# Optimization experiments

Hardware: AMD Instinct MI355X
Metric: run time of the kernel (lower is better)

## Reference

```python
import jax, jax.numpy as jnp
import numpy as np

NUM_EXPERTS = 64
HIDDEN_DIM = 4096
TOPK = 8


def setup_inputs() -> dict:
    key = jax.random.key(0)
    kx, kw = jax.random.split(key)
    x = jax.random.normal(kx, (16384, HIDDEN_DIM), dtype=jnp.float32)
    # nn.Linear weight is [num_experts, hidden_dim], init N(0, 0.01)
    W = jax.random.normal(kw, (NUM_EXPERTS, HIDDEN_DIM), dtype=jnp.float32) * 0.01
    return {"x": x, "W": W}


def reference(x, W):
    # router logits: [T, E]
    router_logits = jnp.einsum('th,eh->te', x, W)
    score = jnp.clip(router_logits, -2.0, 2.0)
    # top-k over experts (no router_bias branch)
    topk_scores, topk_indices = jax.lax.top_k(score, TOPK)  # [T, K]
    topk_probs = jax.nn.softmax(topk_scores, axis=-1)
    # dispatch index computation (counting-sort style)
    flat = topk_indices.reshape(-1)                      # [T*K]
    indices = jnp.argsort(flat, stable=True).astype(jnp.int32)
    tokens_per_expert = jnp.bincount(flat, length=NUM_EXPERTS)
    group_indices = jnp.cumsum(tokens_per_expert).astype(jnp.int32)
    tokens_per_expert_f = tokens_per_expert.astype(jnp.float32)
    # load-balance loss
    mean_tokens = tokens_per_expert_f / tokens_per_expert_f.sum()
    mean_prob = jax.nn.softmax(router_logits, axis=-1).mean(axis=0)
    lb_loss = jnp.dot(mean_tokens, mean_prob) * NUM_EXPERTS
    # z-loss
    zl = jnp.mean(jax.scipy.special.logsumexp(router_logits, axis=-1) ** 2)
    return (router_logits, topk_probs, topk_indices, group_indices,
            indices, tokens_per_expert, lb_loss, zl)
```

## Files before the change

### kernel.cpp

```cpp
#include <hip/hip_runtime.h>
#include <hip/hip_bf16.h>
#include <math.h>

#define NTOK   16384
#define NEXP   64
#define HID    4096
#define KSEL   8
#define EPS    7.5e-5f
#define NSPLIT 4
#define KSZ    (HID / NSPLIT)

typedef __attribute__((ext_vector_type(8))) short short8;
typedef __attribute__((ext_vector_type(4))) float f32x4;

#define O_LOGITS 0u
#define O_PROBS  1048576u
#define O_TIDX   1179648u
#define O_GROUP  1310720u
#define O_IDX    1310784u
#define O_TPE    1441856u
#define O_LB     1441920u
#define O_ZL     1441921u

#define W_CQ      0u
#define W_GCOUNT  2048u
#define W_OFFS2   4096u
#define W_LSQP    8192u
#define W_LIST    16384u
#define W_PSUM    81920u
#define W_FLAT    262144u
#define W_WF      1048576u
#define W_PART    2097152u
#define PART_STRIDE 1048576ull

__device__ __forceinline__ unsigned short f2bf(float f) {
  unsigned u = __float_as_uint(f);
  return (unsigned short)((u + 0x7fffu + ((u >> 16) & 1u)) >> 16);
}

__device__ __forceinline__ void gload16(const void* g, void* l) {
  __builtin_amdgcn_global_load_lds((const __attribute__((address_space(1))) unsigned int*)g,
                                   (__attribute__((address_space(3))) unsigned int*)l, 16, 0, 0);
}

__global__ __launch_bounds__(256) void k_prep(const float* __restrict__ w,
                                              short8* __restrict__ wf,
                                              int* __restrict__ cq,
                                              int* __restrict__ gcount) {
  const int kk   = blockIdx.x;
  const int nb   = threadIdx.x >> 6;
  const int lane = threadIdx.x & 63;
  const int n    = nb * 16 + (lane & 15);
  const int kb   = kk * 32 + (lane >> 4) * 8;
  const float4* wp = (const float4*)(w + (size_t)n * HID + kb);
  float4 f0 = wp[0], f1 = wp[1];
  float fv[8] = {f0.x, f0.y, f0.z, f0.w, f1.x, f1.y, f1.z, f1.w};
  short8 hi, lo;
#pragma unroll
  for (int j = 0; j < 8; ++j) {
    unsigned short h = f2bf(fv[j]);
    hi[j] = (short)h;
    float r = fv[j] - __uint_as_float((unsigned)h << 16);
    lo[j] = (short)f2bf(r);
  }
  size_t base = ((size_t)(kk * 4 + nb) * 2) * 64 + lane;
  wf[base] = hi;
  wf[base + 64] = lo;
  if (blockIdx.x == 0) {
    cq[threadIdx.x] = 0;
    cq[threadIdx.x + 256] = 0;
    if (threadIdx.x == 0) gcount[0] = 0;
  }
}

__global__ __launch_bounds__(256, 4) void k_gemm(const float* __restrict__ x,
                                                 const short8* __restrict__ wf,
                                                 float* __restrict__ part) {
  __shared__ short8 wl[2][512];
  const int tid  = threadIdx.x;
  const int wv   = tid >> 6;
  const int lane = tid & 63;
  const int t0   = blockIdx.x * 64;
  const int k0   = blockIdx.y * KSZ;
  const int row  = t0 + wv * 16 + (lane & 15);

  const float* xp = x + (size_t)row * HID + k0 + (lane >> 4) * 8;
  const short8* wbase = wf + (size_t)(k0 >> 5) * 512;

  auto stage = [&](int c, int b) {
    const short8* src = wbase + (size_t)c * 512;
#pragma unroll
    for (int r = 0; r < 2; ++r) {
      const int o = r * 256 + wv * 64;
      gload16(src + o + lane, &wl[b][o]);
    }
  };

  f32x4 acc[4] = {{0,0,0,0},{0,0,0,0},{0,0,0,0},{0,0,0,0}};

  stage(0, 0);
  __syncthreads();
  const int nch = KSZ >> 5;
  for (int c = 0; c < nch; ++c) {
    const int b = c & 1;
    if (c + 1 < nch) stage(c + 1, b ^ 1);

    const float4* xq = (const float4*)(xp + c * 32);
    float4 f0 = xq[0], f1 = xq[1];
    unsigned xb[8] = {__float_as_uint(f0.x), __float_as_uint(f0.y),
                      __float_as_uint(f0.z), __float_as_uint(f0.w),
                      __float_as_uint(f1.x), __float_as_uint(f1.y),
                      __float_as_uint(f1.z), __float_as_uint(f1.w)};
    union { unsigned u[4]; short8 s; } ua, ul;
#pragma unroll
    for (int p = 0; p < 4; ++p) {
      unsigned b0 = xb[2 * p], b1 = xb[2 * p + 1];
      ua.u[p] = __builtin_amdgcn_perm(b1, b0, 0x07060302u);
      float r0 = __uint_as_float(b0) - __uint_as_float(b0 & 0xffff0000u);
      float r1 = __uint_as_float(b1) - __uint_as_float(b1 & 0xffff0000u);
      unsigned t0b = __float_as_uint(r0), t1b = __float_as_uint(r1);
      t0b += 0x7fffu + ((t0b >> 16) & 1u);
      t1b += 0x7fffu + ((t1b >> 16) & 1u);
      ul.u[p] = __builtin_amdgcn_perm(t1b, t0b, 0x07060302u);
    }
    short8 ah = ua.s, al = ul.s;

#pragma unroll
    for (int nb = 0; nb < 4; ++nb) {
      short8 bh = wl[b][nb * 128 + lane];
      short8 bl = wl[b][nb * 128 + 64 + lane];
      acc[nb] = __builtin_amdgcn_mfma_f32_16x16x32_bf16(ah, bh, acc[nb], 0, 0, 0);
      acc[nb] = __builtin_amdgcn_mfma_f32_16x16x32_bf16(al, bh, acc[nb], 0, 0, 0);
      acc[nb] = __builtin_amdgcn_mfma_f32_16x16x32_bf16(ah, bl, acc[nb], 0, 0, 0);
    }
    __syncthreads();
  }

  float* p = part + (size_t)blockIdx.y * PART_STRIDE;
  const int mrow = t0 + wv * 16 + (lane >> 4) * 4;
  const int col  = lane & 15;
#pragma unroll
  for (int nb = 0; nb < 4; ++nb)
#pragma unroll
    for (int r = 0; r < 4; ++r)
      p[(size_t)(mrow + r) * 64 + nb * 16 + col] = acc[nb][r];
}

__global__ __launch_bounds__(256) void k_rowtail(const float* __restrict__ part,
                                                 float* __restrict__ out,
                                                 int* __restrict__ cq,
                                                 float* __restrict__ psum,
                                                 float* __restrict__ lsqp,
                                                 int* __restrict__ gcount,
                                                 int* __restrict__ list,
                                                 int* __restrict__ flat) {
  __shared__ float tile[64][68];
  __shared__ float rmv[64], invv[64];
  __shared__ int   hist[64];
  const int bid  = blockIdx.x;
  const int tid  = threadIdx.x;
  const int wv   = tid >> 6;
  const int lane = tid & 63;
  const int t0   = bid * 64;
  if (tid < 64) hist[tid] = 0;

  {
    const size_t boff = (size_t)bid * 4096;
#pragma unroll
    for (int k = 0; k < 16; ++k) {
      int idx = k * 256 + tid;
      float v = part[boff + idx];
#pragma unroll
      for (int s = 1; s < NSPLIT; ++s) v += part[(size_t)s * PART_STRIDE + boff + idx];
      tile[idx >> 6][idx & 63] = v;
      out[O_LOGITS + boff + idx] = v;
    }
  }
  __syncthreads();

  if (wv == 1) {
    const int r = lane;
    float rm = -3.0e38f;
#pragma unroll
    for (int c4 = 0; c4 < 16; ++c4) {
      float4 f = *(float4*)&tile[r][c4 * 4];
      rm = fmaxf(rm, fmaxf(fmaxf(f.x, f.y), fmaxf(f.z, f.w)));
    }
    float se = 0.0f;
#pragma unroll
    for (int c4 = 0; c4 < 16; ++c4) {
      float4 f = *(float4*)&tile[r][c4 * 4];
      se += expf(f.x - rm) + expf(f.y - rm) + expf(f.z - rm) + expf(f.w - rm);
    }
    rmv[r] = rm; invv[r] = 1.0f / se;
    float lse = rm + logf(se);
    float l2 = lse * lse;
#pragma unroll
    for (int o = 32; o > 0; o >>= 1) l2 += __shfl_down(l2, o);
    if (lane == 0) lsqp[bid] = l2;
  }
  __syncthreads();

  if (wv == 0) {
    const unsigned t = t0 + lane;
    float val[9]; int idx[9];
#pragma unroll
    for (int j = 0; j < 9; ++j) { val[j] = -3.0e38f; idx[j] = 0; }
    bool flag = false;
#pragma unroll
    for (int c4 = 0; c4 < 16; ++c4) {
      float4 f = *(float4*)&tile[lane][c4 * 4];
      float fe[4] = {f.x, f.y, f.z, f.w};
#pragma unroll
      for (int jj = 0; jj < 4; ++jj) {
        float v = fe[jj];
        flag = flag || (fabsf(fabsf(v) - 2.0f) < EPS);
        float c = fminf(fmaxf(v, -2.0f), 2.0f);
        int id = c4 * 4 + jj;
#pragma unroll
        for (int j = 0; j < 9; ++j) {
          bool sw = c > val[j];
          float tv = sw ? val[j] : c; int ti = sw ? idx[j] : id;
          val[j] = sw ? c : val[j];   idx[j] = sw ? id : idx[j];
          c = tv; id = ti;
        }
      }
    }
#pragma unroll
    for (int j = 0; j < 8; ++j) {
      float gap = val[j] - val[j + 1];
      bool bothclip = (val[j] == val[j + 1]) && (fabsf(val[j]) == 2.0f);
      flag = flag || (gap < EPS && !bothclip);
    }
    if (!flag) {
      float m = val[0], pe[8], sum = 0.0f;
#pragma unroll
      for (int j = 0; j < 8; ++j) { pe[j] = expf(val[j] - m); sum += pe[j]; }
      float inv = 1.0f / sum;
      *(float4*)&out[O_PROBS + (size_t)t * 8]     = make_float4(pe[0]*inv, pe[1]*inv, pe[2]*inv, pe[3]*inv);
      *(float4*)&out[O_PROBS + (size_t)t * 8 + 4] = make_float4(pe[4]*inv, pe[5]*inv, pe[6]*inv, pe[7]*inv);
      *(float4*)&out[O_TIDX + (size_t)t * 8]      = make_float4((float)idx[0], (float)idx[1], (float)idx[2], (float)idx[3]);
      *(float4*)&out[O_TIDX + (size_t)t * 8 + 4]  = make_float4((float)idx[4], (float)idx[5], (float)idx[6], (float)idx[7]);
      *(int4*)&flat[(size_t)t * 8]     = make_int4(idx[0], idx[1], idx[2], idx[3]);
      *(int4*)&flat[(size_t)t * 8 + 4] = make_int4(idx[4], idx[5], idx[6], idx[7]);
#pragma unroll
      for (int j = 0; j < 8; ++j) atomicAdd(&hist[idx[j]], 1);
    } else {
      int sl = atomicAdd(gcount, 1);
      list[sl] = (int)t;
    }
  } else if (wv == 2 || wv == 3) {
    const int e = lane, half = wv - 2;
    float s = 0.0f;
#pragma unroll
    for (int r = 0; r < 32; ++r) {
      int rr = half * 32 + r;
      s += expf(tile[rr][e] - rmv[rr]) * invv[rr];
    }
    psum[(size_t)bid * 128 + half * 64 + e] = s;
  }
  __syncthreads();
  if (tid < 64) atomicAdd(&cq[(bid >> 5) * 64 + tid], hist[tid]);
}

__global__ __launch_bounds__(256) void k_repair(const float* __restrict__ x,
                                                const float* __restrict__ w,
                                                const int* __restrict__ list,
                                                const int* __restrict__ gcount,
                                                float* __restrict__ out,
                                                int* __restrict__ cq,
                                                int* __restrict__ flat) {
  __shared__ double sh[4][64];
  __shared__ double tot[64];
  const int tid = threadIdx.x;
  const int wave = tid >> 6, lane = tid & 63;
  const int n = *gcount;
  for (int i = blockIdx.x; i < n; i += 256) {
    const int row = list[i];
    const float* xr = x + (size_t)row * HID;
    const float* wr = w + (size_t)lane * HID;
    double p0 = 0.0, p1 = 0.0, p2 = 0.0, p3 = 0.0;
    const int kb = wave * 1024;
    for (int k = kb; k < kb + 1024; k += 4) {
      float4 xv = *(const float4*)&xr[k];
      float4 wv = *(const float4*)&wr[k];
      p0 = fma((double)xv.x, (double)wv.x, p0);
      p1 = fma((double)xv.y, (double)wv.y, p1);
      p2 = fma((double)xv.z, (double)wv.z, p2);
      p3 = fma((double)xv.w, (double)wv.w, p3);
    }
    sh[wave][lane] = (p0 + p1) + (p2 + p3);
    __syncthreads();
    if (wave == 0) tot[lane] = (sh[0][lane] + sh[1][lane]) + (sh[2][lane] + sh[3][lane]);
    __syncthreads();
    if (tid == 0) {
      double val[8]; int idx[8];
#pragma unroll
      for (int j = 0; j < 8; ++j) { val[j] = -1.0e300; idx[j] = 0; }
      for (int e = 0; e < 64; ++e) {
        double c = fmin(fmax(tot[e], -2.0), 2.0);
        int id = e;
#pragma unroll
        for (int j = 0; j < 8; ++j) {
          bool sw = c > val[j];
          double tv = sw ? val[j] : c; int ti = sw ? idx[j] : id;
          val[j] = sw ? c : val[j];    idx[j] = sw ? id : idx[j];
          c = tv; id = ti;
        }
      }
      float m = (float)val[0], pe[8], sum = 0.0f;
#pragma unroll
      for (int j = 0; j < 8; ++j) { pe[j] = expf((float)val[j] - m); sum += pe[j]; }
      float inv = 1.0f / sum;
      const int q = row >> 11;
#pragma unroll
      for (int j = 0; j < 8; ++j) {
        out[O_PROBS + (size_t)row * 8 + j] = pe[j] * inv;
        out[O_TIDX  + (size_t)row * 8 + j] = (float)idx[j];
        flat[(size_t)row * 8 + j] = idx[j];
        atomicAdd(&cq[q * 64 + idx[j]], 1);
      }
    }
    __syncthreads();
  }
}

__global__ __launch_bounds__(256) void k_final(const int* __restrict__ cq,
                                               const float* __restrict__ psum,
                                               const float* __restrict__ lsqp,
                                               float* __restrict__ out,
                                               int* __restrict__ offs2) {
  __shared__ int   ctot[64];
  __shared__ float gsum[4][64];
  const int tid = threadIdx.x;
  const int e = tid & 63, g = tid >> 6;

  if (tid < 64) {
    int tpe = 0;
#pragma unroll
    for (int q = 0; q < 8; ++q) tpe += cq[q * 64 + tid];
    ctot[tid] = tpe;
  }
  float ps = 0.0f;
  for (int b = g; b < 256; b += 4) ps += psum[(size_t)b * 128 + e] + psum[(size_t)b * 128 + 64 + e];
  gsum[g][e] = ps;
  __syncthreads();

  if (tid < 64) {
    int incl = 0;
    for (int i = 0; i <= tid; ++i) incl += ctot[i];
    int tpe = ctot[tid];
    out[O_TPE + tid]   = (float)tpe;
    out[O_GROUP + tid] = (float)incl;
    int o = incl - tpe;
#pragma unroll
    for (int q = 0; q < 8; ++q) { offs2[tid * 8 + q] = o; o += cq[q * 64 + tid]; }

    float pst = (gsum[0][tid] + gsum[1][tid]) + (gsum[2][tid] + gsum[3][tid]);
    float term = ((float)tpe / 131072.0f) * (pst / 16384.0f) * 64.0f;
#pragma unroll
    for (int o2 = 32; o2 > 0; o2 >>= 1) term += __shfl_down(term, o2);
    float zs = (lsqp[tid * 4] + lsqp[tid * 4 + 1]) + (lsqp[tid * 4 + 2] + lsqp[tid * 4 + 3]);
#pragma unroll
    for (int o2 = 32; o2 > 0; o2 >>= 1) zs += __shfl_down(zs, o2);
    if (tid == 0) { out[O_LB] = term; out[O_ZL] = zs / 16384.0f; }
  }
}

__global__ __launch_bounds__(256) void k_dispatch(const int* __restrict__ flat,
                                                  const int* __restrict__ offs2,
                                                  float* __restrict__ out) {
  __shared__ int wcs[4];
  const int e = blockIdx.x >> 3;
  const int q = blockIdx.x & 7;
  const int tid = threadIdx.x;
  const int lane = tid & 63;
  const int wv = tid >> 6;
  int base = offs2[e * 8 + q];
  const int seg0 = q * 16384;
  for (int c0 = 0; c0 < 16384; c0 += 2048) {
    const int j0 = seg0 + c0 + tid * 8;
    const int4* f4 = reinterpret_cast<const int4*>(flat + j0);
    int4 a = f4[0], b = f4[1];
    int v[8] = {a.x, a.y, a.z, a.w, b.x, b.y, b.z, b.w};
    int mcnt = 0;
#pragma unroll
    for (int k = 0; k < 8; ++k) mcnt += (v[k] == e) ? 1 : 0;
    int sc = mcnt;
#pragma unroll
    for (int o = 1; o < 64; o <<= 1) {
      int nn = __shfl_up(sc, o);
      if (lane >= o) sc += nn;
    }
    int excl = sc - mcnt;
    if (lane == 63) wcs[wv] = sc;
    __syncthreads();
    int woff = 0, tot = 0;
#pragma unroll
    for (int i = 0; i < 4; ++i) { int ci = wcs[i]; woff += (i < wv) ? ci : 0; tot += ci; }
    int pos = base + woff + excl;
#pragma unroll
    for (int k = 0; k < 8; ++k) {
      if (v[k] == e) { out[O_IDX + pos] = (float)(j0 + k); pos++; }
    }
    base += tot;
    __syncthreads();
  }
}

extern "C" void kernel_launch(void* const* d_in, const int* in_sizes, int n_in,
                              void* d_out, int out_size, void* d_ws, size_t ws_size,
                              hipStream_t stream) {
  (void)in_sizes; (void)n_in; (void)out_size; (void)ws_size;
  const float* x  = (const float*)d_in[0];
  const float* Wm = (const float*)d_in[1];
  float* out = (float*)d_out;
  char*  ws  = (char*)d_ws;

  int*    cq     = (int*)(ws + W_CQ);
  int*    gcount = (int*)(ws + W_GCOUNT);
  int*    offs2  = (int*)(ws + W_OFFS2);
  float*  lsqp   = (float*)(ws + W_LSQP);
  int*    list   = (int*)(ws + W_LIST);
  float*  psum   = (float*)(ws + W_PSUM);
  int*    flat   = (int*)(ws + W_FLAT);
  short8* wf     = (short8*)(ws + W_WF);
  float*  part   = (float*)(ws + W_PART);

  k_prep    <<<dim3(128), dim3(256), 0, stream>>>(Wm, wf, cq, gcount);
  k_gemm    <<<dim3(NTOK / 64, NSPLIT), dim3(256), 0, stream>>>(x, wf, part);
  k_rowtail <<<dim3(256), dim3(256), 0, stream>>>(part, out, cq, psum, lsqp, gcount, list, flat);
  k_repair  <<<dim3(256), dim3(256), 0, stream>>>(x, Wm, list, gcount, out, cq, flat);
  k_final   <<<dim3(1),   dim3(256), 0, stream>>>(cq, psum, lsqp, out, offs2);
  k_dispatch<<<dim3(512), dim3(256), 0, stream>>>(flat, offs2, out);
}
```

Before: 169.7 us.

## Process two 64-row tiles per GEMM block and double the K-split

Each GEMM block now handles 128 token rows as two 64-row sub-tiles that share every staged chunk of weight fragments in LDS. The K dimension is split eight ways instead of four, so the grid keeps the same number of blocks. The aim is to reuse each LDS weight load twice and to keep more independent global loads of x in flight per wave. The cost is twice the accumulator registers and twice as many partial-sum slices that must be written out and then reduced by the row-tail kernel.

```diff
diff --git a/kernel.cpp b/kernel.cpp
--- a/kernel.cpp
+++ b/kernel.cpp
@@ -7,7 +7,7 @@
 #define HID    4096
 #define KSEL   8
 #define EPS    7.5e-5f
-#define NSPLIT 4
+#define NSPLIT 8
 #define KSZ    (HID / NSPLIT)
 
 typedef __attribute__((ext_vector_type(8))) short short8;
@@ -80,11 +80,12 @@
   const int tid  = threadIdx.x;
   const int wv   = tid >> 6;
   const int lane = tid & 63;
-  const int t0   = blockIdx.x * 64;
+  const int t0   = blockIdx.x * 128;
   const int k0   = blockIdx.y * KSZ;
-  const int row  = t0 + wv * 16 + (lane & 15);
-
-  const float* xp = x + (size_t)row * HID + k0 + (lane >> 4) * 8;
+  const int rowA = t0 + wv * 16 + (lane & 15);
+
+  const float* xpA = x + (size_t)rowA * HID + k0 + (lane >> 4) * 8;
+  const float* xpB = xpA + (size_t)64 * HID;
   const short8* wbase = wf + (size_t)(k0 >> 5) * 512;
 
   auto stage = [&](int c, int b) {
@@ -96,15 +97,7 @@
     }
   };
 
-  f32x4 acc[4] = {{0,0,0,0},{0,0,0,0},{0,0,0,0},{0,0,0,0}};
-
-  stage(0, 0);
-  __syncthreads();
-  const int nch = KSZ >> 5;
-  for (int c = 0; c < nch; ++c) {
-    const int b = c & 1;
-    if (c + 1 < nch) stage(c + 1, b ^ 1);
-
+  auto split = [&](const float* xp, int c, short8& ah, short8& al) {
     const float4* xq = (const float4*)(xp + c * 32);
     float4 f0 = xq[0], f1 = xq[1];
     unsigned xb[8] = {__float_as_uint(f0.x), __float_as_uint(f0.y),
@@ -123,27 +116,47 @@
       t1b += 0x7fffu + ((t1b >> 16) & 1u);
       ul.u[p] = __builtin_amdgcn_perm(t1b, t0b, 0x07060302u);
     }
-    short8 ah = ua.s, al = ul.s;
+    ah = ua.s; al = ul.s;
+  };
+
+  f32x4 accA[4] = {{0,0,0,0},{0,0,0,0},{0,0,0,0},{0,0,0,0}};
+  f32x4 accB[4] = {{0,0,0,0},{0,0,0,0},{0,0,0,0},{0,0,0,0}};
+
+  const int nch = KSZ >> 5;
+  stage(0, 0);
+  __syncthreads();
+  for (int c = 0; c < nch; ++c) {
+    const int b = c & 1;
+    if (c + 1 < nch) stage(c + 1, b ^ 1);
+
+    short8 ahA, alA, ahB, alB;
+    split(xpA, c, ahA, alA);
+    split(xpB, c, ahB, alB);
 
 #pragma unroll
     for (int nb = 0; nb < 4; ++nb) {
       short8 bh = wl[b][nb * 128 + lane];
       short8 bl = wl[b][nb * 128 + 64 + lane];
-      acc[nb] = __builtin_amdgcn_mfma_f32_16x16x32_bf16(ah, bh, acc[nb], 0, 0, 0);
-      acc[nb] = __builtin_amdgcn_mfma_f32_16x16x32_bf16(al, bh, acc[nb], 0, 0, 0);
-      acc[nb] = __builtin_amdgcn_mfma_f32_16x16x32_bf16(ah, bl, acc[nb], 0, 0, 0);
+      accA[nb] = __builtin_amdgcn_mfma_f32_16x16x32_bf16(ahA, bh, accA[nb], 0, 0, 0);
+      accA[nb] = __builtin_amdgcn_mfma_f32_16x16x32_bf16(alA, bh, accA[nb], 0, 0, 0);
+      accA[nb] = __builtin_amdgcn_mfma_f32_16x16x32_bf16(ahA, bl, accA[nb], 0, 0, 0);
+      accB[nb] = __builtin_amdgcn_mfma_f32_16x16x32_bf16(ahB, bh, accB[nb], 0, 0, 0);
+      accB[nb] = __builtin_amdgcn_mfma_f32_16x16x32_bf16(alB, bh, accB[nb], 0, 0, 0);
+      accB[nb] = __builtin_amdgcn_mfma_f32_16x16x32_bf16(ahB, bl, accB[nb], 0, 0, 0);
     }
     __syncthreads();
   }
 
   float* p = part + (size_t)blockIdx.y * PART_STRIDE;
-  const int mrow = t0 + wv * 16 + (lane >> 4) * 4;
-  const int col  = lane & 15;
+  const int mrowA = t0 + wv * 16 + (lane >> 4) * 4;
+  const int col   = lane & 15;
 #pragma unroll
   for (int nb = 0; nb < 4; ++nb)
 #pragma unroll
-    for (int r = 0; r < 4; ++r)
-      p[(size_t)(mrow + r) * 64 + nb * 16 + col] = acc[nb][r];
+    for (int r = 0; r < 4; ++r) {
+      p[(size_t)(mrowA + r) * 64 + nb * 16 + col]      = accA[nb][r];
+      p[(size_t)(mrowA + 64 + r) * 64 + nb * 16 + col] = accB[nb][r];
+    }
 }
 
 __global__ __launch_bounds__(256) void k_rowtail(const float* __restrict__ part,
@@ -428,7 +441,7 @@
   float*  part   = (float*)(ws + W_PART);
 
   k_prep    <<<dim3(128), dim3(256), 0, stream>>>(Wm, wf, cq, gcount);
-  k_gemm    <<<dim3(NTOK / 64, NSPLIT), dim3(256), 0, stream>>>(x, wf, part);
+  k_gemm    <<<dim3(NTOK / 128, NSPLIT), dim3(256), 0, stream>>>(x, wf, part);
   k_rowtail <<<dim3(256), dim3(256), 0, stream>>>(part, out, cq, psum, lsqp, gcount, list, flat);
   k_repair  <<<dim3(256), dim3(256), 0, stream>>>(x, Wm, list, gcount, out, cq, flat);
   k_final   <<<dim3(1),   dim3(256), 0, stream>>>(cq, psum, lsqp, out, offs2);
```

Result: slower. 173.8 us (+2.4%).

## Fold repair into rowtail with candidate-only fp64 recompute; merge final into dispatch

Applied to the files above, without the earlier changes.

Rows whose top-k is ambiguous are now recomputed inside the row-tail kernel. Only the candidate experts within a margin of the 9th value get an fp64 dot product, each split across the lanes of a wavefront. The finalize kernel is merged into dispatch: every dispatch block recomputes the per-expert totals and its own base offset, and block 0 writes the losses. This drops two kernel launches plus the global flag list and counter. The cost is serialized per-row repair loops inside rowtail blocks and redundant prefix sums in every dispatch block.

```diff
diff --git a/kernel.cpp b/kernel.cpp
--- a/kernel.cpp
+++ b/kernel.cpp
@@ -23,10 +23,7 @@
 #define O_ZL     1441921u
 
 #define W_CQ      0u
-#define W_GCOUNT  2048u
-#define W_OFFS2   4096u
 #define W_LSQP    8192u
-#define W_LIST    16384u
 #define W_PSUM    81920u
 #define W_FLAT    262144u
 #define W_WF      1048576u
@@ -45,8 +42,7 @@
 
 __global__ __launch_bounds__(256) void k_prep(const float* __restrict__ w,
                                               short8* __restrict__ wf,
-                                              int* __restrict__ cq,
-                                              int* __restrict__ gcount) {
+                                              int* __restrict__ cq) {
   const int kk   = blockIdx.x;
   const int nb   = threadIdx.x >> 6;
   const int lane = threadIdx.x & 63;
@@ -69,7 +65,6 @@
   if (blockIdx.x == 0) {
     cq[threadIdx.x] = 0;
     cq[threadIdx.x + 256] = 0;
-    if (threadIdx.x == 0) gcount[0] = 0;
   }
 }
 
@@ -147,22 +142,27 @@
 }
 
 __global__ __launch_bounds__(256) void k_rowtail(const float* __restrict__ part,
+                                                 const float* __restrict__ x,
+                                                 const float* __restrict__ w,
                                                  float* __restrict__ out,
                                                  int* __restrict__ cq,
                                                  float* __restrict__ psum,
                                                  float* __restrict__ lsqp,
-                                                 int* __restrict__ gcount,
-                                                 int* __restrict__ list,
                                                  int* __restrict__ flat) {
   __shared__ float tile[64][68];
-  __shared__ float rmv[64], invv[64];
+  __shared__ float rmv[64], invv[64], val8s[64];
   __shared__ int   hist[64];
+  __shared__ int   fl_rows[64];
+  __shared__ int   fl_n;
+  __shared__ unsigned long long candmask;
+  __shared__ double cexact[64];
   const int bid  = blockIdx.x;
   const int tid  = threadIdx.x;
   const int wv   = tid >> 6;
   const int lane = tid & 63;
   const int t0   = bid * 64;
   if (tid < 64) hist[tid] = 0;
+  if (tid == 0) fl_n = 0;
 
   {
     const size_t boff = (size_t)bid * 4096;
@@ -226,6 +226,7 @@
         }
       }
     }
+    val8s[lane] = val[8];
 #pragma unroll
     for (int j = 0; j < 8; ++j) {
       float gap = val[j] - val[j + 1];
@@ -246,8 +247,8 @@
 #pragma unroll
       for (int j = 0; j < 8; ++j) atomicAdd(&hist[idx[j]], 1);
     } else {
-      int sl = atomicAdd(gcount, 1);
-      list[sl] = (int)t;
+      int sl = atomicAdd(&fl_n, 1);
+      fl_rows[sl] = lane;
     }
   } else if (wv == 2 || wv == 3) {
     const int e = lane, half = wv - 2;
@@ -260,45 +261,51 @@
     psum[(size_t)bid * 128 + half * 64 + e] = s;
   }
   __syncthreads();
-  if (tid < 64) atomicAdd(&cq[(bid >> 5) * 64 + tid], hist[tid]);
-}
-
-__global__ __launch_bounds__(256) void k_repair(const float* __restrict__ x,
-                                                const float* __restrict__ w,
-                                                const int* __restrict__ list,
-                                                const int* __restrict__ gcount,
-                                                float* __restrict__ out,
-                                                int* __restrict__ cq,
-                                                int* __restrict__ flat) {
-  __shared__ double sh[4][64];
-  __shared__ double tot[64];
-  const int tid = threadIdx.x;
-  const int wave = tid >> 6, lane = tid & 63;
-  const int n = *gcount;
-  for (int i = blockIdx.x; i < n; i += 256) {
-    const int row = list[i];
-    const float* xr = x + (size_t)row * HID;
-    const float* wr = w + (size_t)lane * HID;
-    double p0 = 0.0, p1 = 0.0, p2 = 0.0, p3 = 0.0;
-    const int kb = wave * 1024;
-    for (int k = kb; k < kb + 1024; k += 4) {
-      float4 xv = *(const float4*)&xr[k];
-      float4 wv = *(const float4*)&wr[k];
-      p0 = fma((double)xv.x, (double)wv.x, p0);
-      p1 = fma((double)xv.y, (double)wv.y, p1);
-      p2 = fma((double)xv.z, (double)wv.z, p2);
-      p3 = fma((double)xv.w, (double)wv.w, p3);
-    }
-    sh[wave][lane] = (p0 + p1) + (p2 + p3);
-    __syncthreads();
-    if (wave == 0) tot[lane] = (sh[0][lane] + sh[1][lane]) + (sh[2][lane] + sh[3][lane]);
-    __syncthreads();
-    if (tid == 0) {
+
+  for (int i = 0; i < fl_n; ++i) {
+    const int r = fl_rows[i];
+    if (wv == 0) {
+      float c = fminf(fmaxf(tile[r][lane], -2.0f), 2.0f);
+      bool cnd = (c >= val8s[r] - 3.0f * EPS);
+      unsigned long long m = __ballot(cnd);
+      if (lane == 0) candmask = m;
+    }
+    __syncthreads();
+    const unsigned long long m = candmask;
+    const float* xr = x + (size_t)(t0 + r) * HID;
+    {
+      int ord = 0;
+      for (int e = 0; e < 64; ++e) {
+        if ((m >> e) & 1ull) {
+          if ((ord & 3) == wv) {
+            const float* wr = w + (size_t)e * HID;
+            double p0 = 0.0, p1 = 0.0, p2 = 0.0, p3 = 0.0;
+            const int kb = lane * 64;
+            for (int k = kb; k < kb + 64; k += 4) {
+              float4 xv = *(const float4*)&xr[k];
+              float4 wv4 = *(const float4*)&wr[k];
+              p0 = fma((double)xv.x, (double)wv4.x, p0);
+              p1 = fma((double)xv.y, (double)wv4.y, p1);
+              p2 = fma((double)xv.z, (double)wv4.z, p2);
+              p3 = fma((double)xv.w, (double)wv4.w, p3);
+            }
+            double p = (p0 + p1) + (p2 + p3);
+#pragma unroll
+            for (int o = 32; o > 0; o >>= 1) p += __shfl_down(p, o);
+            if (lane == 0) cexact[e] = fmin(fmax(p, -2.0), 2.0);
+          }
+          ord++;
+        }
+      }
+    }
+    __syncthreads();
+    if (tid == r) {
       double val[8]; int idx[8];
 #pragma unroll
       for (int j = 0; j < 8; ++j) { val[j] = -1.0e300; idx[j] = 0; }
       for (int e = 0; e < 64; ++e) {
-        double c = fmin(fmax(tot[e], -2.0), 2.0);
+        if (!((m >> e) & 1ull)) continue;
+        double c = cexact[e];
         int id = e;
 #pragma unroll
         for (int j = 0; j < 8; ++j) {
@@ -308,75 +315,79 @@
           c = tv; id = ti;
         }
       }
-      float m = (float)val[0], pe[8], sum = 0.0f;
-#pragma unroll
-      for (int j = 0; j < 8; ++j) { pe[j] = expf((float)val[j] - m); sum += pe[j]; }
+      float mm = (float)val[0], pe[8], sum = 0.0f;
+#pragma unroll
+      for (int j = 0; j < 8; ++j) { pe[j] = expf((float)val[j] - mm); sum += pe[j]; }
       float inv = 1.0f / sum;
-      const int q = row >> 11;
+      const unsigned t = t0 + r;
 #pragma unroll
       for (int j = 0; j < 8; ++j) {
-        out[O_PROBS + (size_t)row * 8 + j] = pe[j] * inv;
-        out[O_TIDX  + (size_t)row * 8 + j] = (float)idx[j];
-        flat[(size_t)row * 8 + j] = idx[j];
-        atomicAdd(&cq[q * 64 + idx[j]], 1);
+        out[O_PROBS + (size_t)t * 8 + j] = pe[j] * inv;
+        out[O_TIDX  + (size_t)t * 8 + j] = (float)idx[j];
+        flat[(size_t)t * 8 + j] = idx[j];
+        atomicAdd(&hist[idx[j]], 1);
       }
     }
     __syncthreads();
   }
-}
-
-__global__ __launch_bounds__(256) void k_final(const int* __restrict__ cq,
-                                               const float* __restrict__ psum,
-                                               const float* __restrict__ lsqp,
-                                               float* __restrict__ out,
-                                               int* __restrict__ offs2) {
-  __shared__ int   ctot[64];
+
+  if (tid < 64) atomicAdd(&cq[(bid >> 5) * 64 + tid], hist[tid]);
+}
+
+__global__ __launch_bounds__(256) void k_dispatch(const int* __restrict__ flat,
+                                                  const int* __restrict__ cq,
+                                                  const float* __restrict__ psum,
+                                                  const float* __restrict__ lsqp,
+                                                  float* __restrict__ out) {
+  __shared__ int ctot[64];
+  __shared__ int sbase;
+  __shared__ int wcs[4];
   __shared__ float gsum[4][64];
-  const int tid = threadIdx.x;
-  const int e = tid & 63, g = tid >> 6;
-
-  if (tid < 64) {
-    int tpe = 0;
-#pragma unroll
-    for (int q = 0; q < 8; ++q) tpe += cq[q * 64 + tid];
-    ctot[tid] = tpe;
-  }
-  float ps = 0.0f;
-  for (int b = g; b < 256; b += 4) ps += psum[(size_t)b * 128 + e] + psum[(size_t)b * 128 + 64 + e];
-  gsum[g][e] = ps;
-  __syncthreads();
-
-  if (tid < 64) {
-    int incl = 0;
-    for (int i = 0; i <= tid; ++i) incl += ctot[i];
-    int tpe = ctot[tid];
-    out[O_TPE + tid]   = (float)tpe;
-    out[O_GROUP + tid] = (float)incl;
-    int o = incl - tpe;
-#pragma unroll
-    for (int q = 0; q < 8; ++q) { offs2[tid * 8 + q] = o; o += cq[q * 64 + tid]; }
-
-    float pst = (gsum[0][tid] + gsum[1][tid]) + (gsum[2][tid] + gsum[3][tid]);
-    float term = ((float)tpe / 131072.0f) * (pst / 16384.0f) * 64.0f;
-#pragma unroll
-    for (int o2 = 32; o2 > 0; o2 >>= 1) term += __shfl_down(term, o2);
-    float zs = (lsqp[tid * 4] + lsqp[tid * 4 + 1]) + (lsqp[tid * 4 + 2] + lsqp[tid * 4 + 3]);
-#pragma unroll
-    for (int o2 = 32; o2 > 0; o2 >>= 1) zs += __shfl_down(zs, o2);
-    if (tid == 0) { out[O_LB] = term; out[O_ZL] = zs / 16384.0f; }
-  }
-}
-
-__global__ __launch_bounds__(256) void k_dispatch(const int* __restrict__ flat,
-                                                  const int* __restrict__ offs2,
-                                                  float* __restrict__ out) {
-  __shared__ int wcs[4];
   const int e = blockIdx.x >> 3;
   const int q = blockIdx.x & 7;
   const int tid = threadIdx.x;
   const int lane = tid & 63;
   const int wv = tid >> 6;
-  int base = offs2[e * 8 + q];
+
+  if (tid < 64) {
+    int tpe = 0;
+#pragma unroll
+    for (int qq = 0; qq < 8; ++qq) tpe += cq[qq * 64 + tid];
+    ctot[tid] = tpe;
+  }
+  __syncthreads();
+  if (tid == 0) {
+    int b = 0;
+    for (int i = 0; i < e; ++i) b += ctot[i];
+    for (int qq = 0; qq < q; ++qq) b += cq[qq * 64 + e];
+    sbase = b;
+  }
+
+  if (blockIdx.x == 0) {
+    const int e2 = tid & 63, g = tid >> 6;
+    float ps = 0.0f;
+    for (int b = g; b < 256; b += 4) ps += psum[(size_t)b * 128 + e2] + psum[(size_t)b * 128 + 64 + e2];
+    gsum[g][e2] = ps;
+    __syncthreads();
+    if (tid < 64) {
+      int incl = 0;
+      for (int i = 0; i <= tid; ++i) incl += ctot[i];
+      int tpe = ctot[tid];
+      out[O_TPE + tid]   = (float)tpe;
+      out[O_GROUP + tid] = (float)incl;
+      float pst = (gsum[0][tid] + gsum[1][tid]) + (gsum[2][tid] + gsum[3][tid]);
+      float term = ((float)tpe / 131072.0f) * (pst / 16384.0f) * 64.0f;
+#pragma unroll
+      for (int o2 = 32; o2 > 0; o2 >>= 1) term += __shfl_down(term, o2);
+      float zs = (lsqp[tid * 4] + lsqp[tid * 4 + 1]) + (lsqp[tid * 4 + 2] + lsqp[tid * 4 + 3]);
+#pragma unroll
+      for (int o2 = 32; o2 > 0; o2 >>= 1) zs += __shfl_down(zs, o2);
+      if (tid == 0) { out[O_LB] = term; out[O_ZL] = zs / 16384.0f; }
+    }
+  }
+  __syncthreads();
+
+  int base = sbase;
   const int seg0 = q * 16384;
   for (int c0 = 0; c0 < 16384; c0 += 2048) {
     const int j0 = seg0 + c0 + tid * 8;
@@ -418,19 +429,14 @@
   char*  ws  = (char*)d_ws;
 
   int*    cq     = (int*)(ws + W_CQ);
-  int*    gcount = (int*)(ws + W_GCOUNT);
-  int*    offs2  = (int*)(ws + W_OFFS2);
   float*  lsqp   = (float*)(ws + W_LSQP);
-  int*    list   = (int*)(ws + W_LIST);
   float*  psum   = (float*)(ws + W_PSUM);
   int*    flat   = (int*)(ws + W_FLAT);
   short8* wf     = (short8*)(ws + W_WF);
   float*  part   = (float*)(ws + W_PART);
 
-  k_prep    <<<dim3(128), dim3(256), 0, stream>>>(Wm, wf, cq, gcount);
+  k_prep    <<<dim3(128), dim3(256), 0, stream>>>(Wm, wf, cq);
   k_gemm    <<<dim3(NTOK / 64, NSPLIT), dim3(256), 0, stream>>>(x, wf, part);
-  k_rowtail <<<dim3(256), dim3(256), 0, stream>>>(part, out, cq, psum, lsqp, gcount, list, flat);
-  k_repair  <<<dim3(256), dim3(256), 0, stream>>>(x, Wm, list, gcount, out, cq, flat);
-  k_final   <<<dim3(1),   dim3(256), 0, stream>>>(cq, psum, lsqp, out, offs2);
-  k_dispatch<<<dim3(512), dim3(256), 0, stream>>>(flat, offs2, out);
-}
+  k_rowtail <<<dim3(256), dim3(256), 0, stream>>>(part, x, Wm, out, cq, psum, lsqp, flat);
+  k_dispatch<<<dim3(512), dim3(256), 0, stream>>>(flat, cq, psum, lsqp, out);
+}
```

After: 155.5 us. 8.4% less time.
